# Kernel optimization log

Hardware: AMD Instinct MI355X
Metric: run time of the kernel (lower is better)

The kernel has to match this reference:

```python
import jax, jax.numpy as jnp
import numpy as np

N_NODES = 100000
N_EDGES = 1600000
IN_CH = 64
HID = 128
N_CLASSES = 10
N_GRAPHS = 64


def setup_inputs() -> dict:
    key = jax.random.key(0)
    ks = jax.random.split(key, 10)
    x = jax.random.normal(ks[0], (N_NODES, IN_CH), dtype=jnp.float32)
    edge_index = jax.random.randint(ks[1], (2, N_EDGES), 0, N_NODES, dtype=jnp.int64)
    batch = jnp.sort(jax.random.randint(ks[2], (N_NODES,), 0, N_GRAPHS, dtype=jnp.int64))
    # GCNConv / Linear parameters (glorot-ish scaling)
    W1 = jax.random.normal(ks[3], (IN_CH, HID), dtype=jnp.float32) * (1.0 / np.sqrt(IN_CH))
    b1 = jnp.zeros((HID,), dtype=jnp.float32)
    W2 = jax.random.normal(ks[4], (HID, HID), dtype=jnp.float32) * (1.0 / np.sqrt(HID))
    b2 = jnp.zeros((HID,), dtype=jnp.float32)
    Wc = jax.random.normal(ks[5], (HID, N_CLASSES), dtype=jnp.float32) * (1.0 / np.sqrt(HID))
    bc = jnp.zeros((N_CLASSES,), dtype=jnp.float32)
    return {"x": x, "W1": W1, "b1": b1, "W2": W2, "b2": b2,
            "Wc": Wc, "bc": bc, "edge_index": edge_index, "batch": batch}


def reference(x, W1, b1, W2, b2, Wc, bc, edge_index, batch):
    N = x.shape[0]
    # add self-loops (PyG GCNConv default)
    loop = jnp.arange(N, dtype=edge_index.dtype)
    src = jnp.concatenate([edge_index[0], loop])  # message sources (j)
    dst = jnp.concatenate([edge_index[1], loop])  # aggregation targets (i)
    # symmetric normalization D^{-1/2} (A+I) D^{-1/2}
    deg = jax.ops.segment_sum(jnp.ones_like(dst, dtype=x.dtype), dst, num_segments=N)
    dinv = jnp.where(deg > 0, jax.lax.rsqrt(jnp.maximum(deg, 1e-12)), 0.0)
    norm = dinv[src] * dinv[dst]  # [E+N]

    def gcn_conv(h, W, b):
        h = h @ W  # transform first, then aggregate (gather-scale-scatter)
        msg = h[src] * norm[:, None]
        return jax.ops.segment_sum(msg, dst, num_segments=N) + b

    h = jax.nn.relu(gcn_conv(x, W1, b1))
    h = jax.nn.relu(gcn_conv(h, W2, b2))
    # global mean pool over graphs
    cnt = jax.ops.segment_sum(jnp.ones((N,), x.dtype), batch, num_segments=N_GRAPHS)
    pooled = jax.ops.segment_sum(h, batch, num_segments=N_GRAPHS) / jnp.maximum(cnt, 1.0)[:, None]
    return pooled @ Wc + bc
```

## Files before the change

### kernel.cpp

```cpp
#include <hip/hip_runtime.h>

#define NN 100000
#define NE 1600000

#define BSHIFT 9
#define NBKT 256
#define BCAP 12288
#define TILE 4096

using half8 = __attribute__((ext_vector_type(8))) _Float16;
using f32x4 = __attribute__((ext_vector_type(4))) float;

__device__ inline unsigned short f2bf(float f) {
    unsigned int u = __float_as_uint(f);
    unsigned int r = (u + 0x7fffu + ((u >> 16) & 1u)) >> 16;
    return (unsigned short)r;
}
__device__ inline float bf2f(unsigned short h) {
    return __uint_as_float(((unsigned int)h) << 16);
}
__device__ inline float bflo(unsigned int v) { return __uint_as_float(v << 16); }
__device__ inline float bfhi(unsigned int v) { return __uint_as_float(v & 0xffff0000u); }
__device__ inline unsigned short f2h(float f) {
    union { _Float16 h; unsigned short u; } c; c.h = (_Float16)f; return c.u;
}

__global__ __launch_bounds__(256) void k_bucket(
    const int* __restrict__ src, const int* __restrict__ dst,
    int* __restrict__ gcnt, unsigned* __restrict__ stage, int E) {
    __shared__ unsigned st[TILE];
    __shared__ unsigned char stb[TILE];
    __shared__ int hist4[4 * NBKT];
    __shared__ int hist[NBKT];
    __shared__ int s[NBKT];
    __shared__ int offs[NBKT];
    __shared__ int cursor[NBKT];
    __shared__ int gbase[NBKT];
    int tid = threadIdx.x;
    int wv = tid >> 6;
    int t0 = blockIdx.x * TILE;
    int m = E - t0; if (m > TILE) m = TILE;

    for (int i = tid; i < 4 * NBKT; i += 256) hist4[i] = 0;
    __syncthreads();
    for (int i = tid; i < m; i += 256)
        atomicAdd(&hist4[wv * NBKT + (dst[t0 + i] >> BSHIFT)], 1);
    __syncthreads();
    int h = hist4[tid] + hist4[NBKT + tid] + hist4[2 * NBKT + tid] + hist4[3 * NBKT + tid];
    hist[tid] = h;
    s[tid] = h;
    __syncthreads();
    for (int off = 1; off < NBKT; off <<= 1) {
        int t = (tid >= off) ? s[tid - off] : 0;
        __syncthreads();
        s[tid] += t;
        __syncthreads();
    }
    offs[tid] = s[tid] - hist[tid];
    cursor[tid] = s[tid] - hist[tid];
    gbase[tid] = atomicAdd(&gcnt[tid], hist[tid]);
    __syncthreads();
    for (int i = tid; i < m; i += 256) {
        int d = dst[t0 + i];
        int b = d >> BSHIFT;
        unsigned packed = ((unsigned)src[t0 + i] << BSHIFT) | (unsigned)(d & 511);
        int pos = atomicAdd(&cursor[b], 1);
        st[pos] = packed;
        stb[pos] = (unsigned char)b;
    }
    __syncthreads();
    for (int i = tid; i < m; i += 256) {
        int b = stb[i];
        int idx = gbase[b] + (i - offs[b]);
        if (idx < BCAP) stage[(size_t)b * BCAP + idx] = st[i];
    }
}

__global__ __launch_bounds__(512) void k_cnt_bucket(
    const unsigned* __restrict__ stage, const int* __restrict__ gcnt,
    int* __restrict__ cnt, float* __restrict__ dinv, int N) {
    __shared__ int h[512];
    int b = blockIdx.x;
    int tid = threadIdx.x;
    h[tid] = 0;
    __syncthreads();
    int n = gcnt[b]; if (n > BCAP) n = BCAP;
    const unsigned* sg = stage + (size_t)b * BCAP;
    for (int i = tid; i < n; i += 512)
        atomicAdd(&h[sg[i] & 511], 1);
    __syncthreads();
    int d = (b << BSHIFT) | tid;
    if (d < N) {
        cnt[d] = h[tid];
        dinv[d] = rsqrtf((float)(h[tid] + 1));
    }
}

__global__ void k_scan1(const int* __restrict__ cnt, int* __restrict__ excl,
                        int* __restrict__ bsums, int N) {
    __shared__ int s[512];
    int tid = threadIdx.x;
    int i = blockIdx.x * 512 + tid;
    int v = (i < N) ? cnt[i] : 0;
    s[tid] = v;
    __syncthreads();
    for (int off = 1; off < 512; off <<= 1) {
        int t = (tid >= off) ? s[tid - off] : 0;
        __syncthreads();
        s[tid] += t;
        __syncthreads();
    }
    if (i < N) excl[i] = s[tid] - v;
    if (tid == 511) bsums[blockIdx.x] = s[511];
}

__global__ void k_scan2(int* __restrict__ bsums, int nb) {
    if (blockIdx.x == 0 && threadIdx.x == 0) {
        int run = 0;
        for (int b = 0; b < nb; ++b) { int t = bsums[b]; bsums[b] = run; run += t; }
    }
}

__global__ void k_scan3(int* __restrict__ row_ptr, const int* __restrict__ bsums,
                        int N, int E) {
    int i = blockIdx.x * blockDim.x + threadIdx.x;
    if (i < N) row_ptr[i] += bsums[i >> 9];
    if (i == 0) row_ptr[N] = E;
}

__global__ __launch_bounds__(512) void k_scatter(
    const unsigned* __restrict__ stage, const int* __restrict__ gcnt,
    const int* __restrict__ row_ptr, int* __restrict__ col, int N) {
    __shared__ int cur[512];
    int b = blockIdx.x;
    int tid = threadIdx.x;
    int d0 = (b << BSHIFT) | tid;
    cur[tid] = (d0 < N) ? row_ptr[d0] : 0;
    __syncthreads();
    int n = gcnt[b]; if (n > BCAP) n = BCAP;
    const unsigned* sg = stage + (size_t)b * BCAP;
    for (int i = tid; i < n; i += 512) {
        unsigned e = sg[i];
        int pos = atomicAdd(&cur[e & 511], 1);
        col[pos] = (int)(e >> BSHIFT);
    }
}

__global__ void k_toscaled(const float* __restrict__ in, const float* __restrict__ dinv,
                           unsigned short* __restrict__ out, int n8) {
    int i = blockIdx.x * blockDim.x + threadIdx.x;
    if (i >= n8) return;
    float di = dinv[i >> 3];
    const float4* p = (const float4*)(in + (size_t)i * 8);
    float4 a = p[0], b = p[1];
    uint4 o;
    o.x = (unsigned)f2bf(di * a.x) | ((unsigned)f2bf(di * a.y) << 16);
    o.y = (unsigned)f2bf(di * a.z) | ((unsigned)f2bf(di * a.w) << 16);
    o.z = (unsigned)f2bf(di * b.x) | ((unsigned)f2bf(di * b.y) << 16);
    o.w = (unsigned)f2bf(di * b.z) | ((unsigned)f2bf(di * b.w) << 16);
    ((uint4*)out)[i] = o;
}

__global__ void k_packW(const float* __restrict__ W, half8* __restrict__ wpack, int K) {
    int t = blockIdx.x * blockDim.x + threadIdx.x;
    int total = (K / 32) * 8 * 64;
    if (t >= total) return;
    int s = t >> 9;
    int j = (t >> 6) & 7;
    int l = t & 63;
    half8 hv;
#pragma unroll
    for (int jj = 0; jj < 8; ++jj)
        hv[jj] = (_Float16)W[(size_t)(32 * s + 8 * (l >> 4) + jj) * 128 + 16 * j + (l & 15)];
    wpack[t] = hv;
}


template <int C>
__global__ void k_agg(const unsigned short* __restrict__ xb, const int* __restrict__ row_ptr,
                      const int* __restrict__ col, const float* __restrict__ dinv,
                      unsigned short* __restrict__ out, int N) {
    int node = blockIdx.x * (blockDim.x >> 6) + (threadIdx.x >> 6);
    int lane = threadIdx.x & 63;
    if (node >= N) return;
    int beg = row_ptr[node], end = row_ptr[node + 1];
    float di = dinv[node];

    if constexpr (C == 64) {
        float acc = bf2f(xb[(size_t)node * 64 + lane]);
        for (int base = beg; base < end; base += 64) {
            int m = end - base; if (m > 64) m = 64;
            int sel = (lane < m) ? lane : (m - 1);
            int cl = col[base + sel];
            int k = 0;
            for (; k + 8 <= m; k += 8) {
                int c0 = __shfl(cl, k),     c1 = __shfl(cl, k + 1);
                int c2 = __shfl(cl, k + 2), c3 = __shfl(cl, k + 3);
                int c4 = __shfl(cl, k + 4), c5 = __shfl(cl, k + 5);
                int c6 = __shfl(cl, k + 6), c7 = __shfl(cl, k + 7);
                unsigned short v0 = xb[(size_t)c0 * 64 + lane];
                unsigned short v1 = xb[(size_t)c1 * 64 + lane];
                unsigned short v2 = xb[(size_t)c2 * 64 + lane];
                unsigned short v3 = xb[(size_t)c3 * 64 + lane];
                unsigned short v4 = xb[(size_t)c4 * 64 + lane];
                unsigned short v5 = xb[(size_t)c5 * 64 + lane];
                unsigned short v6 = xb[(size_t)c6 * 64 + lane];
                unsigned short v7 = xb[(size_t)c7 * 64 + lane];
                acc += bf2f(v0) + bf2f(v1) + bf2f(v2) + bf2f(v3)
                     + bf2f(v4) + bf2f(v5) + bf2f(v6) + bf2f(v7);
            }
            for (; k < m; ++k) {
                int c = __shfl(cl, k);
                acc += bf2f(xb[(size_t)c * 64 + lane]);
            }
        }
        out[(size_t)node * 64 + lane] = f2h(di * acc);
    } else {
        const unsigned int* xb2 = (const unsigned int*)xb;
        unsigned int sv = xb2[(size_t)node * 64 + lane];
        float ax = bflo(sv), ay = bfhi(sv);
        for (int base = beg; base < end; base += 64) {
            int m = end - base; if (m > 64) m = 64;
            int sel = (lane < m) ? lane : (m - 1);
            int cl = col[base + sel];
            int k = 0;
            for (; k + 8 <= m; k += 8) {
                int c0 = __shfl(cl, k),     c1 = __shfl(cl, k + 1);
                int c2 = __shfl(cl, k + 2), c3 = __shfl(cl, k + 3);
                int c4 = __shfl(cl, k + 4), c5 = __shfl(cl, k + 5);
                int c6 = __shfl(cl, k + 6), c7 = __shfl(cl, k + 7);
                unsigned int v0 = xb2[(size_t)c0 * 64 + lane];
                unsigned int v1 = xb2[(size_t)c1 * 64 + lane];
                unsigned int v2 = xb2[(size_t)c2 * 64 + lane];
                unsigned int v3 = xb2[(size_t)c3 * 64 + lane];
                unsigned int v4 = xb2[(size_t)c4 * 64 + lane];
                unsigned int v5 = xb2[(size_t)c5 * 64 + lane];
                unsigned int v6 = xb2[(size_t)c6 * 64 + lane];
                unsigned int v7 = xb2[(size_t)c7 * 64 + lane];
                ax += bflo(v0) + bflo(v1) + bflo(v2) + bflo(v3)
                    + bflo(v4) + bflo(v5) + bflo(v6) + bflo(v7);
                ay += bfhi(v0) + bfhi(v1) + bfhi(v2) + bfhi(v3)
                    + bfhi(v4) + bfhi(v5) + bfhi(v6) + bfhi(v7);
            }
            for (; k < m; ++k) {
                int c = __shfl(cl, k);
                unsigned int v = xb2[(size_t)c * 64 + lane];
                ax += bflo(v);
                ay += bfhi(v);
            }
        }
        ((unsigned int*)out)[(size_t)node * 64 + lane] =
            (unsigned int)f2h(di * ax) | ((unsigned int)f2h(di * ay) << 16);
    }
}


template <int K, bool SCALE>
__global__ __launch_bounds__(256) void k_gemm_mfma(
    const unsigned short* __restrict__ A, const half8* __restrict__ wpack,
    const float* __restrict__ bias, const float* __restrict__ dinv,
    unsigned short* __restrict__ outp, int N) {
    int lane = threadIdx.x & 63;
    int wave = threadIdx.x >> 6;
    int row0 = blockIdx.x * 64 + wave * 16;
    int ar = row0 + (lane & 15);
    if (ar >= N) ar = N - 1;
    const _Float16* Ah = (const _Float16*)A;

    f32x4 acc[8];
#pragma unroll
    for (int j = 0; j < 8; ++j) acc[j] = (f32x4)(0.f);

#pragma unroll
    for (int s = 0; s < K / 32; ++s) {
        half8 av = *(const half8*)(Ah + (size_t)ar * K + 32 * s + 8 * (lane >> 4));
#pragma unroll
        for (int j = 0; j < 8; ++j) {
            half8 bv = wpack[(s * 8 + j) * 64 + lane];
            acc[j] = __builtin_amdgcn_mfma_f32_16x16x32_f16(av, bv, acc[j], 0, 0, 0);
        }
    }

    int rowb = row0 + (lane >> 4) * 4;
    float dv[4];
#pragma unroll
    for (int r = 0; r < 4; ++r) {
        int rr = rowb + r; if (rr >= N) rr = N - 1;
        dv[r] = SCALE ? dinv[rr] : 1.f;
    }
#pragma unroll
    for (int j = 0; j < 8; ++j) {
        int colc = j * 16 + (lane & 15);
        float b = bias[colc];
#pragma unroll
        for (int r = 0; r < 4; ++r) {
            int rr = rowb + r;
            if (rr < N) {
                float v = fmaxf(acc[j][r] + b, 0.f);
                if constexpr (SCALE) v *= dv[r];
                outp[(size_t)rr * 128 + colc] = f2bf(v);
            }
        }
    }
}


__global__ void k_cntg_bs(const int* __restrict__ batch, int* __restrict__ cntg, int N) {
    int g = threadIdx.x;
    if (g >= 64) return;
    int lo = 0, hi = N;
    while (lo < hi) { int mid = (lo + hi) >> 1; if (batch[mid] < g) lo = mid + 1; else hi = mid; }
    int start = lo;
    lo = 0; hi = N;
    while (lo < hi) { int mid = (lo + hi) >> 1; if (batch[mid] < g + 1) lo = mid + 1; else hi = mid; }
    cntg[g] = lo - start;
}

#define POOL_NPB 64
__global__ void k_pool(const unsigned short* __restrict__ h, const int* __restrict__ batch,
                       float* __restrict__ pooled, int N) {
    int tid = threadIdx.x;
    int start = blockIdx.x * POOL_NPB;
    int end = start + POOL_NPB;
    if (end > N) end = N;
    if (start >= end) return;
    int curg = batch[start];
    float acc = 0.f;
    for (int n = start; n < end; ++n) {
        int g = batch[n];
        if (g != curg) {
            atomicAdd(&pooled[curg * 128 + tid], acc);
            acc = 0.f;
            curg = g;
        }
        acc += bf2f(h[(size_t)n * 128 + tid]);
    }
    atomicAdd(&pooled[curg * 128 + tid], acc);
}

__global__ void k_final(const float* __restrict__ pooled, const int* __restrict__ cntg,
                        const float* __restrict__ Wc, const float* __restrict__ bc,
                        float* __restrict__ out) {
    for (int idx = threadIdx.x; idx < 64 * 10; idx += 256) {
        int g = idx / 10, c = idx % 10;
        float s = 0.f;
        for (int k = 0; k < 128; ++k) s += pooled[g * 128 + k] * Wc[k * 10 + c];
        float cnt = (float)cntg[g];
        if (cnt < 1.f) cnt = 1.f;
        out[idx] = s / cnt + bc[c];
    }
}


extern "C" void kernel_launch(void* const* d_in, const int* in_sizes, int n_in,
                              void* d_out, int out_size, void* d_ws, size_t ws_size,
                              hipStream_t stream) {
    const float* x  = (const float*)d_in[0];
    const float* W1 = (const float*)d_in[1];
    const float* b1 = (const float*)d_in[2];
    const float* W2 = (const float*)d_in[3];
    const float* b2 = (const float*)d_in[4];
    const float* Wc = (const float*)d_in[5];
    const float* bc = (const float*)d_in[6];
    const int* ei   = (const int*)d_in[7];
    const int* batch = (const int*)d_in[8];

    const int E = in_sizes[7] / 2;
    const int N = in_sizes[8];
    const int* src = ei;
    const int* dst = ei + E;

    char* p = (char*)d_ws;
    auto alloc = [&](size_t bytes) -> void* {
        void* r = (void*)p;
        p += (bytes + 255) & ~(size_t)255;
        return r;
    };
    int*   cnt      = (int*)alloc((size_t)N * 4);
    float* dinv     = (float*)alloc((size_t)N * 4);
    int*   row_ptr  = (int*)alloc((size_t)(N + 1) * 4);
    int*   bsums    = (int*)alloc(4096);
    int*   col      = (int*)alloc((size_t)E * 4);
    int*   gcnt     = (int*)alloc(NBKT * 4);
    unsigned* stage = (unsigned*)alloc((size_t)NBKT * BCAP * 4);
    unsigned short* xb    = (unsigned short*)alloc((size_t)N * 64 * 2);
    unsigned short* h1b   = (unsigned short*)alloc((size_t)N * 128 * 2);
    unsigned short* aggb1 = (unsigned short*)alloc((size_t)N * 64 * 2);
    unsigned short* aggb2 = (unsigned short*)alloc((size_t)N * 128 * 2);
    unsigned short* h2b   = (unsigned short*)alloc((size_t)N * 128 * 2);
    half8* w1p      = (half8*)alloc(1024 * 16);
    half8* w2p      = (half8*)alloc(2048 * 16);
    float* pooled   = (float*)alloc(64 * 128 * 4);
    int*   cntg     = (int*)alloc(64 * 4);

    hipMemsetAsync(gcnt, 0, NBKT * 4, stream);
    hipMemsetAsync(pooled, 0, 64 * 128 * 4, stream);

    int nb = (N + 511) / 512;

    k_bucket<<<(E + TILE - 1) / TILE, 256, 0, stream>>>(src, dst, gcnt, stage, E);
    k_cnt_bucket<<<nb, 512, 0, stream>>>(stage, gcnt, cnt, dinv, N);
    k_scan1<<<nb, 512, 0, stream>>>(cnt, row_ptr, bsums, N);
    k_scan2<<<1, 64, 0, stream>>>(bsums, nb);
    k_scan3<<<(N + 255) / 256, 256, 0, stream>>>(row_ptr, bsums, N, E);
    k_scatter<<<nb, 512, 0, stream>>>(stage, gcnt, row_ptr, col, N);

    k_packW<<<4, 256, 0, stream>>>(W1, w1p, 64);
    k_packW<<<8, 256, 0, stream>>>(W2, w2p, 128);
    k_toscaled<<<(N * 8 + 255) / 256, 256, 0, stream>>>(x, dinv, xb, N * 8);

    k_agg<64><<<(N + 3) / 4, 256, 0, stream>>>(xb, row_ptr, col, dinv, aggb1, N);
    k_gemm_mfma<64, true><<<(N + 63) / 64, 256, 0, stream>>>(aggb1, w1p, b1, dinv, h1b, N);

    k_agg<128><<<(N + 3) / 4, 256, 0, stream>>>(h1b, row_ptr, col, dinv, aggb2, N);
    k_gemm_mfma<128, false><<<(N + 63) / 64, 256, 0, stream>>>(aggb2, w2p, b2, nullptr, h2b, N);

    k_cntg_bs<<<1, 64, 0, stream>>>(batch, cntg, N);
    k_pool<<<(N + POOL_NPB - 1) / POOL_NPB, 128, 0, stream>>>(h2b, batch, pooled, N);
    k_final<<<1, 256, 0, stream>>>(pooled, cntg, Wc, bc, (float*)d_out);
}
```

Baseline: 279.4 us.

## Fuse neighbor aggregation with MFMA GEMM via LDS staging per layer

Merges each layer's gather-aggregation kernel and its MFMA linear transform into one kernel. Each wave aggregates 16 node rows into shared memory, and those rows then feed the MFMA directly, so the intermediate aggregated buffers are no longer written to or re-read from global memory. It also merges the two weight-pack launches and folds the graph-count binary search into the final kernel to cut launch count. The cost is parallelism: one wave now handles 16 nodes serially where each node previously had its own wave, which hurts latency hiding on the irregular gathers.

```diff
diff --git a/kernel.cpp b/kernel.cpp
--- a/kernel.cpp
+++ b/kernel.cpp
@@ -21,9 +21,6 @@
 }
 __device__ inline float bflo(unsigned int v) { return __uint_as_float(v << 16); }
 __device__ inline float bfhi(unsigned int v) { return __uint_as_float(v & 0xffff0000u); }
-__device__ inline unsigned short f2h(float f) {
-    union { _Float16 h; unsigned short u; } c; c.h = (_Float16)f; return c.u;
-}
 
 __global__ __launch_bounds__(256) void k_bucket(
     const int* __restrict__ src, const int* __restrict__ dst,
@@ -161,119 +158,121 @@
     ((uint4*)out)[i] = o;
 }
 
-__global__ void k_packW(const float* __restrict__ W, half8* __restrict__ wpack, int K) {
+__global__ void k_packW(const float* __restrict__ W1, const float* __restrict__ W2,
+                        half8* __restrict__ w1p, half8* __restrict__ w2p) {
     int t = blockIdx.x * blockDim.x + threadIdx.x;
-    int total = (K / 32) * 8 * 64;
-    if (t >= total) return;
-    int s = t >> 9;
-    int j = (t >> 6) & 7;
-    int l = t & 63;
+    const float* W; half8* wp; int tt;
+    if (t < 1024) { W = W1; wp = w1p; tt = t; }
+    else if (t < 3072) { W = W2; wp = w2p; tt = t - 1024; }
+    else return;
+    int s = tt >> 9;
+    int j = (tt >> 6) & 7;
+    int l = tt & 63;
     half8 hv;
 #pragma unroll
     for (int jj = 0; jj < 8; ++jj)
         hv[jj] = (_Float16)W[(size_t)(32 * s + 8 * (l >> 4) + jj) * 128 + 16 * j + (l & 15)];
-    wpack[t] = hv;
-}
-
-
-template <int C>
-__global__ void k_agg(const unsigned short* __restrict__ xb, const int* __restrict__ row_ptr,
-                      const int* __restrict__ col, const float* __restrict__ dinv,
-                      unsigned short* __restrict__ out, int N) {
-    int node = blockIdx.x * (blockDim.x >> 6) + (threadIdx.x >> 6);
-    int lane = threadIdx.x & 63;
-    if (node >= N) return;
-    int beg = row_ptr[node], end = row_ptr[node + 1];
-    float di = dinv[node];
-
-    if constexpr (C == 64) {
-        float acc = bf2f(xb[(size_t)node * 64 + lane]);
-        for (int base = beg; base < end; base += 64) {
-            int m = end - base; if (m > 64) m = 64;
-            int sel = (lane < m) ? lane : (m - 1);
-            int cl = col[base + sel];
-            int k = 0;
-            for (; k + 8 <= m; k += 8) {
-                int c0 = __shfl(cl, k),     c1 = __shfl(cl, k + 1);
-                int c2 = __shfl(cl, k + 2), c3 = __shfl(cl, k + 3);
-                int c4 = __shfl(cl, k + 4), c5 = __shfl(cl, k + 5);
-                int c6 = __shfl(cl, k + 6), c7 = __shfl(cl, k + 7);
-                unsigned short v0 = xb[(size_t)c0 * 64 + lane];
-                unsigned short v1 = xb[(size_t)c1 * 64 + lane];
-                unsigned short v2 = xb[(size_t)c2 * 64 + lane];
-                unsigned short v3 = xb[(size_t)c3 * 64 + lane];
-                unsigned short v4 = xb[(size_t)c4 * 64 + lane];
-                unsigned short v5 = xb[(size_t)c5 * 64 + lane];
-                unsigned short v6 = xb[(size_t)c6 * 64 + lane];
-                unsigned short v7 = xb[(size_t)c7 * 64 + lane];
-                acc += bf2f(v0) + bf2f(v1) + bf2f(v2) + bf2f(v3)
-                     + bf2f(v4) + bf2f(v5) + bf2f(v6) + bf2f(v7);
-            }
-            for (; k < m; ++k) {
-                int c = __shfl(cl, k);
-                acc += bf2f(xb[(size_t)c * 64 + lane]);
-            }
-        }
-        out[(size_t)node * 64 + lane] = f2h(di * acc);
-    } else {
-        const unsigned int* xb2 = (const unsigned int*)xb;
-        unsigned int sv = xb2[(size_t)node * 64 + lane];
-        float ax = bflo(sv), ay = bfhi(sv);
-        for (int base = beg; base < end; base += 64) {
-            int m = end - base; if (m > 64) m = 64;
-            int sel = (lane < m) ? lane : (m - 1);
-            int cl = col[base + sel];
-            int k = 0;
-            for (; k + 8 <= m; k += 8) {
-                int c0 = __shfl(cl, k),     c1 = __shfl(cl, k + 1);
-                int c2 = __shfl(cl, k + 2), c3 = __shfl(cl, k + 3);
-                int c4 = __shfl(cl, k + 4), c5 = __shfl(cl, k + 5);
-                int c6 = __shfl(cl, k + 6), c7 = __shfl(cl, k + 7);
-                unsigned int v0 = xb2[(size_t)c0 * 64 + lane];
-                unsigned int v1 = xb2[(size_t)c1 * 64 + lane];
-                unsigned int v2 = xb2[(size_t)c2 * 64 + lane];
-                unsigned int v3 = xb2[(size_t)c3 * 64 + lane];
-                unsigned int v4 = xb2[(size_t)c4 * 64 + lane];
-                unsigned int v5 = xb2[(size_t)c5 * 64 + lane];
-                unsigned int v6 = xb2[(size_t)c6 * 64 + lane];
-                unsigned int v7 = xb2[(size_t)c7 * 64 + lane];
-                ax += bflo(v0) + bflo(v1) + bflo(v2) + bflo(v3)
-                    + bflo(v4) + bflo(v5) + bflo(v6) + bflo(v7);
-                ay += bfhi(v0) + bfhi(v1) + bfhi(v2) + bfhi(v3)
-                    + bfhi(v4) + bfhi(v5) + bfhi(v6) + bfhi(v7);
-            }
-            for (; k < m; ++k) {
-                int c = __shfl(cl, k);
-                unsigned int v = xb2[(size_t)c * 64 + lane];
-                ax += bflo(v);
-                ay += bfhi(v);
-            }
-        }
-        ((unsigned int*)out)[(size_t)node * 64 + lane] =
-            (unsigned int)f2h(di * ax) | ((unsigned int)f2h(di * ay) << 16);
-    }
+    wp[tt] = hv;
 }
 
 
 template <int K, bool SCALE>
-__global__ __launch_bounds__(256) void k_gemm_mfma(
-    const unsigned short* __restrict__ A, const half8* __restrict__ wpack,
-    const float* __restrict__ bias, const float* __restrict__ dinv,
+__global__ __launch_bounds__(256) void k_fused(
+    const unsigned short* __restrict__ xb, const int* __restrict__ row_ptr,
+    const int* __restrict__ col, const float* __restrict__ dinv,
+    const half8* __restrict__ wpack, const float* __restrict__ bias,
     unsigned short* __restrict__ outp, int N) {
+    constexpr int PAD = 8;
+    __shared__ _Float16 Alds[4][16][K + PAD];
     int lane = threadIdx.x & 63;
     int wave = threadIdx.x >> 6;
     int row0 = blockIdx.x * 64 + wave * 16;
-    int ar = row0 + (lane & 15);
-    if (ar >= N) ar = N - 1;
-    const _Float16* Ah = (const _Float16*)A;
+
+    for (int r = 0; r < 16; ++r) {
+        int node = row0 + r;
+        if (node >= N) {
+            if constexpr (K == 64) Alds[wave][r][lane] = (_Float16)0.f;
+            else { *(unsigned*)&Alds[wave][r][2 * lane] = 0u; }
+            continue;
+        }
+        int beg = row_ptr[node], end = row_ptr[node + 1];
+        float di = dinv[node];
+        if constexpr (K == 64) {
+            float acc = bf2f(xb[(size_t)node * 64 + lane]);
+            for (int base = beg; base < end; base += 64) {
+                int m = end - base; if (m > 64) m = 64;
+                int sel = (lane < m) ? lane : (m - 1);
+                int cl = col[base + sel];
+                int k = 0;
+                for (; k + 8 <= m; k += 8) {
+                    int c0 = __shfl(cl, k),     c1 = __shfl(cl, k + 1);
+                    int c2 = __shfl(cl, k + 2), c3 = __shfl(cl, k + 3);
+                    int c4 = __shfl(cl, k + 4), c5 = __shfl(cl, k + 5);
+                    int c6 = __shfl(cl, k + 6), c7 = __shfl(cl, k + 7);
+                    unsigned short v0 = xb[(size_t)c0 * 64 + lane];
+                    unsigned short v1 = xb[(size_t)c1 * 64 + lane];
+                    unsigned short v2 = xb[(size_t)c2 * 64 + lane];
+                    unsigned short v3 = xb[(size_t)c3 * 64 + lane];
+                    unsigned short v4 = xb[(size_t)c4 * 64 + lane];
+                    unsigned short v5 = xb[(size_t)c5 * 64 + lane];
+                    unsigned short v6 = xb[(size_t)c6 * 64 + lane];
+                    unsigned short v7 = xb[(size_t)c7 * 64 + lane];
+                    acc += bf2f(v0) + bf2f(v1) + bf2f(v2) + bf2f(v3)
+                         + bf2f(v4) + bf2f(v5) + bf2f(v6) + bf2f(v7);
+                }
+                for (; k < m; ++k) {
+                    int c = __shfl(cl, k);
+                    acc += bf2f(xb[(size_t)c * 64 + lane]);
+                }
+            }
+            Alds[wave][r][lane] = (_Float16)(di * acc);
+        } else {
+            const unsigned* xb2 = (const unsigned*)xb;
+            unsigned sv = xb2[(size_t)node * 64 + lane];
+            float ax = bflo(sv), ay = bfhi(sv);
+            for (int base = beg; base < end; base += 64) {
+                int m = end - base; if (m > 64) m = 64;
+                int sel = (lane < m) ? lane : (m - 1);
+                int cl = col[base + sel];
+                int k = 0;
+                for (; k + 8 <= m; k += 8) {
+                    int c0 = __shfl(cl, k),     c1 = __shfl(cl, k + 1);
+                    int c2 = __shfl(cl, k + 2), c3 = __shfl(cl, k + 3);
+                    int c4 = __shfl(cl, k + 4), c5 = __shfl(cl, k + 5);
+                    int c6 = __shfl(cl, k + 6), c7 = __shfl(cl, k + 7);
+                    unsigned v0 = xb2[(size_t)c0 * 64 + lane];
+                    unsigned v1 = xb2[(size_t)c1 * 64 + lane];
+                    unsigned v2 = xb2[(size_t)c2 * 64 + lane];
+                    unsigned v3 = xb2[(size_t)c3 * 64 + lane];
+                    unsigned v4 = xb2[(size_t)c4 * 64 + lane];
+                    unsigned v5 = xb2[(size_t)c5 * 64 + lane];
+                    unsigned v6 = xb2[(size_t)c6 * 64 + lane];
+                    unsigned v7 = xb2[(size_t)c7 * 64 + lane];
+                    ax += bflo(v0) + bflo(v1) + bflo(v2) + bflo(v3)
+                        + bflo(v4) + bflo(v5) + bflo(v6) + bflo(v7);
+                    ay += bfhi(v0) + bfhi(v1) + bfhi(v2) + bfhi(v3)
+                        + bfhi(v4) + bfhi(v5) + bfhi(v6) + bfhi(v7);
+                }
+                for (; k < m; ++k) {
+                    int c = __shfl(cl, k);
+                    unsigned v = xb2[(size_t)c * 64 + lane];
+                    ax += bflo(v);
+                    ay += bfhi(v);
+                }
+            }
+            _Float16 lo = (_Float16)(di * ax), hi = (_Float16)(di * ay);
+            union { _Float16 h[2]; unsigned u; } pk; pk.h[0] = lo; pk.h[1] = hi;
+            *(unsigned*)&Alds[wave][r][2 * lane] = pk.u;
+        }
+    }
+    __syncthreads();
 
     f32x4 acc[8];
 #pragma unroll
     for (int j = 0; j < 8; ++j) acc[j] = (f32x4)(0.f);
-
 #pragma unroll
     for (int s = 0; s < K / 32; ++s) {
-        half8 av = *(const half8*)(Ah + (size_t)ar * K + 32 * s + 8 * (lane >> 4));
+        half8 av = *(const half8*)&Alds[wave][lane & 15][32 * s + 8 * (lane >> 4)];
 #pragma unroll
         for (int j = 0; j < 8; ++j) {
             half8 bv = wpack[(s * 8 + j) * 64 + lane];
@@ -304,17 +303,6 @@
     }
 }
 
-
-__global__ void k_cntg_bs(const int* __restrict__ batch, int* __restrict__ cntg, int N) {
-    int g = threadIdx.x;
-    if (g >= 64) return;
-    int lo = 0, hi = N;
-    while (lo < hi) { int mid = (lo + hi) >> 1; if (batch[mid] < g) lo = mid + 1; else hi = mid; }
-    int start = lo;
-    lo = 0; hi = N;
-    while (lo < hi) { int mid = (lo + hi) >> 1; if (batch[mid] < g + 1) lo = mid + 1; else hi = mid; }
-    cntg[g] = lo - start;
-}
 
 #define POOL_NPB 64
 __global__ void k_pool(const unsigned short* __restrict__ h, const int* __restrict__ batch,
@@ -338,14 +326,26 @@
     atomicAdd(&pooled[curg * 128 + tid], acc);
 }
 
-__global__ void k_final(const float* __restrict__ pooled, const int* __restrict__ cntg,
+__global__ void k_final(const float* __restrict__ pooled, const int* __restrict__ batch,
                         const float* __restrict__ Wc, const float* __restrict__ bc,
-                        float* __restrict__ out) {
-    for (int idx = threadIdx.x; idx < 64 * 10; idx += 256) {
+                        float* __restrict__ out, int N) {
+    __shared__ int cnts[64];
+    int tid = threadIdx.x;
+    if (tid < 64) {
+        int g = tid;
+        int lo = 0, hi = N;
+        while (lo < hi) { int mid = (lo + hi) >> 1; if (batch[mid] < g) lo = mid + 1; else hi = mid; }
+        int start = lo;
+        lo = 0; hi = N;
+        while (lo < hi) { int mid = (lo + hi) >> 1; if (batch[mid] < g + 1) lo = mid + 1; else hi = mid; }
+        cnts[g] = lo - start;
+    }
+    __syncthreads();
+    for (int idx = tid; idx < 64 * 10; idx += 256) {
         int g = idx / 10, c = idx % 10;
         float s = 0.f;
         for (int k = 0; k < 128; ++k) s += pooled[g * 128 + k] * Wc[k * 10 + c];
-        float cnt = (float)cntg[g];
+        float cnt = (float)cnts[g];
         if (cnt < 1.f) cnt = 1.f;
         out[idx] = s / cnt + bc[c];
     }
@@ -383,15 +383,12 @@
     int*   col      = (int*)alloc((size_t)E * 4);
     int*   gcnt     = (int*)alloc(NBKT * 4);
     unsigned* stage = (unsigned*)alloc((size_t)NBKT * BCAP * 4);
-    unsigned short* xb    = (unsigned short*)alloc((size_t)N * 64 * 2);
-    unsigned short* h1b   = (unsigned short*)alloc((size_t)N * 128 * 2);
-    unsigned short* aggb1 = (unsigned short*)alloc((size_t)N * 64 * 2);
-    unsigned short* aggb2 = (unsigned short*)alloc((size_t)N * 128 * 2);
-    unsigned short* h2b   = (unsigned short*)alloc((size_t)N * 128 * 2);
+    unsigned short* xb  = (unsigned short*)alloc((size_t)N * 64 * 2);
+    unsigned short* h1b = (unsigned short*)alloc((size_t)N * 128 * 2);
+    unsigned short* h2b = (unsigned short*)alloc((size_t)N * 128 * 2);
     half8* w1p      = (half8*)alloc(1024 * 16);
     half8* w2p      = (half8*)alloc(2048 * 16);
     float* pooled   = (float*)alloc(64 * 128 * 4);
-    int*   cntg     = (int*)alloc(64 * 4);
 
     hipMemsetAsync(gcnt, 0, NBKT * 4, stream);
     hipMemsetAsync(pooled, 0, 64 * 128 * 4, stream);
@@ -405,17 +402,12 @@
     k_scan3<<<(N + 255) / 256, 256, 0, stream>>>(row_ptr, bsums, N, E);
     k_scatter<<<nb, 512, 0, stream>>>(stage, gcnt, row_ptr, col, N);
 
-    k_packW<<<4, 256, 0, stream>>>(W1, w1p, 64);
-    k_packW<<<8, 256, 0, stream>>>(W2, w2p, 128);
+    k_packW<<<12, 256, 0, stream>>>(W1, W2, w1p, w2p);
     k_toscaled<<<(N * 8 + 255) / 256, 256, 0, stream>>>(x, dinv, xb, N * 8);
 
-    k_agg<64><<<(N + 3) / 4, 256, 0, stream>>>(xb, row_ptr, col, dinv, aggb1, N);
-    k_gemm_mfma<64, true><<<(N + 63) / 64, 256, 0, stream>>>(aggb1, w1p, b1, dinv, h1b, N);
-
-    k_agg<128><<<(N + 3) / 4, 256, 0, stream>>>(h1b, row_ptr, col, dinv, aggb2, N);
-    k_gemm_mfma<128, false><<<(N + 63) / 64, 256, 0, stream>>>(aggb2, w2p, b2, nullptr, h2b, N);
-
-    k_cntg_bs<<<1, 64, 0, stream>>>(batch, cntg, N);
+    k_fused<64, true><<<(N + 63) / 64, 256, 0, stream>>>(xb, row_ptr, col, dinv, w1p, b1, h1b, N);
+    k_fused<128, false><<<(N + 63) / 64, 256, 0, stream>>>(h1b, row_ptr, col, dinv, w2p, b2, h2b, N);
+
     k_pool<<<(N + POOL_NPB - 1) / POOL_NPB, 128, 0, stream>>>(h2b, batch, pooled, N);
-    k_final<<<1, 256, 0, stream>>>(pooled, cntg, Wc, bc, (float*)d_out);
-}
+    k_final<<<1, 256, 0, stream>>>(pooled, batch, Wc, bc, (float*)d_out, N);
+}
```

New measurement: 349.0 us. 1.25x slower.
